# Kernel optimization log

Hardware: AMD Instinct MI355X
Metric: run time of the kernel (lower is better)

The kernel has to match this reference:

```python
import jax, jax.numpy as jnp
import numpy as np

B, S, D = 4, 2048, 512
QKD = 256
HID = 3 * D  # expansion_factor=3
EPS = 1e-5


def _ln(x, g, b):
    m = jnp.mean(x, axis=-1, keepdims=True)
    v = jnp.mean((x - m) ** 2, axis=-1, keepdims=True)
    return (x - m) * jax.lax.rsqrt(v + EPS) * g + b


def setup_inputs() -> dict:
    key = jax.random.key(0)
    ks = jax.random.split(key, 12)
    s = lambda fan: 1.0 / np.sqrt(fan)
    return {
        "x":  jax.random.normal(ks[0], (B, S, D), jnp.float32),
        "Wm": jax.random.uniform(ks[1], (D, D), jnp.float32, -s(D), s(D)),
        "bm": jnp.zeros((D,), jnp.float32),
        "g1": jnp.ones((D,), jnp.float32),
        "b1": jnp.zeros((D,), jnp.float32),
        "Wh": jax.random.uniform(ks[2], (2 * HID, D), jnp.float32, -s(D), s(D)),
        "bh": jnp.zeros((2 * HID,), jnp.float32),
        "Wq": jax.random.uniform(ks[3], (QKD, D), jnp.float32, -s(D), s(D)),
        "bq": jnp.zeros((QKD,), jnp.float32),
        "Wb": jax.random.normal(ks[4], (QKD, QKD), jnp.float32),
        "Wo": jax.random.uniform(ks[5], (D, HID), jnp.float32, -s(HID), s(HID)),
        "bo": jnp.zeros((D,), jnp.float32),
        "g2": jnp.ones((D,), jnp.float32),
        "b2": jnp.zeros((D,), jnp.float32),
    }


def reference(x, Wm, bm, g1, b1, Wh, bh, Wq, bq, Wb, Wo, bo, g2, b2):
    seq_len = x.shape[-2]
    memory = jnp.einsum('bsd,ed->bse', x, Wm) + bm
    normed = _ln(x + memory, g1, b1)
    h = jax.nn.relu(jnp.einsum('bsd,hd->bsh', normed, Wh) + bh)
    v, gate = h[..., :HID], h[..., HID:]
    Z = jax.nn.relu(jnp.einsum('bsd,qd->bsq', normed, Wq) + bq)  # [B,S,QKD]
    QK = jnp.einsum('bid,de,bje->bij', Z, Wb, Z) / seq_len
    A = jax.nn.relu(QK) ** 2  # relu^2 attention, no softmax
    V = jnp.einsum('bij,bjd->bid', A, v) * gate
    out = _ln(jnp.einsum('bsh,dh->bsd', V, Wo) + bo, g2, b2)
    return out + x
```

## Files before the change

### kernel.cpp

```cpp
#include <hip/hip_runtime.h>

typedef unsigned short u16;
typedef unsigned char u8;
typedef __attribute__((ext_vector_type(8))) short short8;
typedef __attribute__((ext_vector_type(4))) float f32x4;
typedef __attribute__((ext_vector_type(8))) int int8v;
typedef __attribute__((ext_vector_type(4))) int int4v;

#define LN_EPS 1e-5f
#define SCALE_A 4096.f
#define SCALE_V 8.f
#define INV_SCALE_AV (1.f/32768.f)
#define MX_ONE 0x7F7F7F7Fu

__device__ __forceinline__ u16 f2bf(float f){
    union { float f; unsigned u; } c; c.f = f;
    unsigned u = c.u + 0x7FFFu + ((c.u >> 16) & 1u);
    return (u16)(u >> 16);
}
__device__ __forceinline__ float bf2f(u16 h){
    union { unsigned u; float f; } c; c.u = ((unsigned)h) << 16;
    return c.f;
}
__device__ __forceinline__ u8 f2fp8(float f){
    int r = __builtin_amdgcn_cvt_pk_fp8_f32(f, 0.f, 0, false);
    return (u8)(r & 0xFF);
}

enum { EPI_NONE=0, EPI_BIAS_RES, EPI_RELUSQ };
enum { OT_F32=0, OT_BF16=1, OT_FP8=2 };

__device__ __forceinline__ void gl2lds16(const void* g, void* lds){
    __builtin_amdgcn_global_load_lds(
        (const __attribute__((address_space(1))) unsigned*)g,
        (__attribute__((address_space(3))) unsigned*)lds, 16, 0, 0);
}

template<int EPI, int OT>
__global__ __launch_bounds__(256)
void mgemm(const u16* __restrict__ A, const u16* __restrict__ B, void* __restrict__ Cv,
           int K, int lda, int ldb, int ldc,
           long sAb, long sBb, long sCb,
           const float* __restrict__ bias,
           const float* __restrict__ ext, int ldext,
           float scale)
{
    __shared__ u16 sA[2][4096];
    __shared__ u16 sB[2][4096];
    const int tid = threadIdx.x;
    const int m0 = blockIdx.y * 128, n0 = blockIdx.x * 128;
    const int z  = blockIdx.z;
    const u16* Az = A + (size_t)z * sAb;
    const u16* Bz = B + (size_t)z * sBb;

    const int lane = tid & 63, quad = lane >> 4, l15 = lane & 15;
    const int wave = tid >> 6;
    const int wm = (wave >> 1) * 64, wn = (wave & 1) * 64;

    const u16* gA[2]; const u16* gB[2]; int lo[2];
#pragma unroll
    for (int r = 0; r < 2; r++){
        const int c = tid + r * 256;
        gA[r] = Az + (size_t)(m0 + (c & 127)) * lda + (c >> 7) * 8;
        gB[r] = Bz + (size_t)(n0 + (c & 127)) * ldb + (c >> 7) * 8;
        lo[r] = ((tid & 192) + r * 256) * 16;
    }

    auto stage = [&](int buf, int k0){
#pragma unroll
        for (int r = 0; r < 2; r++){
            gl2lds16(gA[r] + k0, (char*)sA[buf] + lo[r]);
            gl2lds16(gB[r] + k0, (char*)sB[buf] + lo[r]);
        }
    };

    f32x4 acc[4][4];
#pragma unroll
    for (int i = 0; i < 4; i++)
#pragma unroll
        for (int j = 0; j < 4; j++) acc[i][j] = (f32x4){0.f,0.f,0.f,0.f};

    stage(0, 0);
    int buf = 0;
    for (int k0 = 0; k0 < K; k0 += 32){
        __syncthreads();
        if (k0 + 32 < K) stage(buf ^ 1, k0 + 32);
        const u16* fA = sA[buf] + quad * 1024 + (wm + l15) * 8;
        const u16* fB = sB[buf] + quad * 1024 + (wn + l15) * 8;
        short8 a[4], b[4];
#pragma unroll
        for (int t = 0; t < 4; t++){
            a[t] = *(const short8*)(fA + t * 128);
            b[t] = *(const short8*)(fB + t * 128);
        }
#pragma unroll
        for (int i = 0; i < 4; i++)
#pragma unroll
            for (int j = 0; j < 4; j++)
                acc[i][j] = __builtin_amdgcn_mfma_f32_16x16x32_bf16(a[i], b[j], acc[i][j], 0, 0, 0);
        buf ^= 1;
    }

    float* Cf = (float*)Cv; u16* Ch = (u16*)Cv; u8* C8 = (u8*)Cv;
    const size_t zc = (size_t)z * sCb;
#pragma unroll
    for (int i = 0; i < 4; i++){
#pragma unroll
        for (int j = 0; j < 4; j++){
            const int n = n0 + wn + j * 16 + l15;
            float bs = (EPI==EPI_BIAS_RES) ? bias[n] : 0.f;
#pragma unroll
            for (int r = 0; r < 4; r++){
                const int m = m0 + wm + i * 16 + quad * 4 + r;
                float v = acc[i][j][r] + bs;
                if (EPI==EPI_BIAS_RES)
                    v += ext[(size_t)m * ldext + n];
                if (EPI==EPI_RELUSQ){ float t = fmaxf(v * scale, 0.f); v = t * t * SCALE_A; }
                if (OT==OT_FP8)       C8[zc + (size_t)m * ldc + n] = f2fp8(v);
                else if (OT==OT_BF16) Ch[zc + (size_t)m * ldc + n] = f2bf(v);
                else                  Cf[zc + (size_t)m * ldc + n] = v;
            }
        }
    }
}

__global__ __launch_bounds__(256)
void mgemm_dual(const u16* __restrict__ Anrm, const u16* __restrict__ Wh,
                const u16* __restrict__ Wq,
                const float* __restrict__ bh, const float* __restrict__ bq,
                u8* __restrict__ v8, u16* __restrict__ gbf, u16* __restrict__ Zb)
{
    __shared__ u16 sA[2][4096];
    __shared__ u16 sB[2][4096];
    const int tid = threadIdx.x;
    const bool isZ = blockIdx.x >= 24;
    const u16* Bm = isZ ? Wq : Wh;
    const float* bias = isZ ? bq : bh;
    const int m0 = blockIdx.y * 128;
    const int n0 = (isZ ? (blockIdx.x - 24) : blockIdx.x) * 128;
    const int K = 512, lda = 512, ldb = 512;

    const int lane = tid & 63, quad = lane >> 4, l15 = lane & 15;
    const int wave = tid >> 6;
    const int wm = (wave >> 1) * 64, wn = (wave & 1) * 64;

    const u16* gA[2]; const u16* gB[2]; int lo[2];
#pragma unroll
    for (int r = 0; r < 2; r++){
        const int c = tid + r * 256;
        gA[r] = Anrm + (size_t)(m0 + (c & 127)) * lda + (c >> 7) * 8;
        gB[r] = Bm   + (size_t)(n0 + (c & 127)) * ldb + (c >> 7) * 8;
        lo[r] = ((tid & 192) + r * 256) * 16;
    }
    auto stage = [&](int buf, int k0){
#pragma unroll
        for (int r = 0; r < 2; r++){
            gl2lds16(gA[r] + k0, (char*)sA[buf] + lo[r]);
            gl2lds16(gB[r] + k0, (char*)sB[buf] + lo[r]);
        }
    };

    f32x4 acc[4][4];
#pragma unroll
    for (int i = 0; i < 4; i++)
#pragma unroll
        for (int j = 0; j < 4; j++) acc[i][j] = (f32x4){0.f,0.f,0.f,0.f};

    stage(0, 0);
    int buf = 0;
    for (int k0 = 0; k0 < K; k0 += 32){
        __syncthreads();
        if (k0 + 32 < K) stage(buf ^ 1, k0 + 32);
        const u16* fA = sA[buf] + quad * 1024 + (wm + l15) * 8;
        const u16* fB = sB[buf] + quad * 1024 + (wn + l15) * 8;
        short8 a[4], b[4];
#pragma unroll
        for (int t = 0; t < 4; t++){
            a[t] = *(const short8*)(fA + t * 128);
            b[t] = *(const short8*)(fB + t * 128);
        }
#pragma unroll
        for (int i = 0; i < 4; i++)
#pragma unroll
            for (int j = 0; j < 4; j++)
                acc[i][j] = __builtin_amdgcn_mfma_f32_16x16x32_bf16(a[i], b[j], acc[i][j], 0, 0, 0);
        buf ^= 1;
    }

#pragma unroll
    for (int i = 0; i < 4; i++){
#pragma unroll
        for (int j = 0; j < 4; j++){
            const int n = n0 + wn + j * 16 + l15;
            const float bs = bias[n];
#pragma unroll
            for (int r = 0; r < 4; r++){
                const int m = m0 + wm + i * 16 + quad * 4 + r;
                float v = fmaxf(acc[i][j][r] + bs, 0.f);
                if (isZ)            Zb[(size_t)m * 256 + n] = f2bf(v);
                else if (n < 1536)  v8[(size_t)m * 1536 + n] = f2fp8(v * SCALE_V);
                else                gbf[(size_t)m * 1536 + n - 1536] = f2bf(v);
            }
        }
    }
}

__global__ __launch_bounds__(256)
void mgemm8mx(const u8* __restrict__ A, const u8* __restrict__ B, u16* __restrict__ C,
              int K, int lda, int ldb, int ldc,
              long sAb, long sBb, long sCb,
              const u16* __restrict__ gate, int ldext, long sEb)
{
    __shared__ u8 sA[16384];
    __shared__ u8 sB[16384];
    const int tid = threadIdx.x;
    const int m0 = blockIdx.y * 128, n0 = blockIdx.x * 128;
    const int z  = blockIdx.z;
    const u8* Az = A + (size_t)z * sAb;
    const u8* Bz = B + (size_t)z * sBb;

    const int lane = tid & 63, quad = lane >> 4, l15 = lane & 15;
    const int wave = tid >> 6;
    const int wm = (wave >> 1) * 64, wn = (wave & 1) * 64;

    const u8* gA[4]; const u8* gB[4]; int lo[4];
#pragma unroll
    for (int p = 0; p < 4; p++){
        const int r = p * 32 + (tid >> 3);
        const int j = (tid & 7) ^ (r & 7);
        gA[p] = Az + (size_t)(m0 + r) * lda + j * 16;
        gB[p] = Bz + (size_t)(n0 + r) * ldb + j * 16;
        lo[p] = p * 4096 + wave * 1024;
    }

    f32x4 acc[4][4];
#pragma unroll
    for (int i = 0; i < 4; i++)
#pragma unroll
        for (int j = 0; j < 4; j++) acc[i][j] = (f32x4){0.f,0.f,0.f,0.f};

    for (int k0 = 0; k0 < K; k0 += 128){
#pragma unroll
        for (int p = 0; p < 4; p++){
            gl2lds16(gA[p] + k0, (char*)sA + lo[p]);
            gl2lds16(gB[p] + k0, (char*)sB + lo[p]);
        }
        __syncthreads();
        int8v a[4], b[4];
#pragma unroll
        for (int i = 0; i < 4; i++){
            const int m = wm + i * 16 + l15;
            const int4v a0 = *(const int4v*)(sA + m * 128 + ((2*quad    ) ^ (m & 7)) * 16);
            const int4v a1 = *(const int4v*)(sA + m * 128 + ((2*quad + 1) ^ (m & 7)) * 16);
            a[i] = (int8v){a0[0],a0[1],a0[2],a0[3],a1[0],a1[1],a1[2],a1[3]};
            const int n = wn + i * 16 + l15;
            const int4v b0 = *(const int4v*)(sB + n * 128 + ((2*quad    ) ^ (n & 7)) * 16);
            const int4v b1 = *(const int4v*)(sB + n * 128 + ((2*quad + 1) ^ (n & 7)) * 16);
            b[i] = (int8v){b0[0],b0[1],b0[2],b0[3],b1[0],b1[1],b1[2],b1[3]};
        }
#pragma unroll
        for (int i = 0; i < 4; i++)
#pragma unroll
            for (int j = 0; j < 4; j++)
                acc[i][j] = __builtin_amdgcn_mfma_scale_f32_16x16x128_f8f6f4(
                    a[i], b[j], acc[i][j], 0, 0, 0, MX_ONE, 0, MX_ONE);
        __syncthreads();
    }

    const size_t zc = (size_t)z * sCb;
#pragma unroll
    for (int i = 0; i < 4; i++){
#pragma unroll
        for (int j = 0; j < 4; j++){
            const int n = n0 + wn + j * 16 + l15;
#pragma unroll
            for (int r = 0; r < 4; r++){
                const int m = m0 + wm + i * 16 + quad * 4 + r;
                float v = acc[i][j][r] * INV_SCALE_AV
                        * bf2f(gate[(size_t)z * sEb + (size_t)m * ldext + n]);
                C[zc + (size_t)m * ldc + n] = f2bf(v);
            }
        }
    }
}

template<bool OUT_BF, bool POST_RES, int NSUM, bool PRE_RES>
__global__ __launch_bounds__(256)
void ln_k(const float* __restrict__ in, const float* __restrict__ g,
          const float* __restrict__ b, const float* __restrict__ res_post,
          const float* __restrict__ res_pre, const float* __restrict__ bias2,
          long pstride, void* __restrict__ out)
{
    const int row = blockIdx.x, tid = threadIdx.x;
    const size_t base = (size_t)row * 512 + tid * 2;
    float2 v = *(const float2*)(in + base);
#pragma unroll
    for (int p = 1; p < NSUM; p++){
        const float2 w = *(const float2*)(in + (size_t)p * pstride + base);
        v.x += w.x; v.y += w.y;
    }
    if (NSUM > 1){
        const float2 bb2 = *(const float2*)(bias2 + tid * 2);
        v.x += bb2.x; v.y += bb2.y;
    }
    if (PRE_RES){
        const float2 r = *(const float2*)(res_pre + base);
        v.x += r.x; v.y += r.y;
    }
    float s = v.x + v.y, ss = v.x * v.x + v.y * v.y;
#pragma unroll
    for (int off = 32; off > 0; off >>= 1){
        s  += __shfl_down(s,  off);
        ss += __shfl_down(ss, off);
    }
    __shared__ float sbuf[8], ssbuf[8];
    const int wid = tid >> 6, lane = tid & 63;
    if (lane == 0){ sbuf[wid] = s; ssbuf[wid] = ss; }
    __syncthreads();
    if (tid == 0){
        float S = 0.f, SS = 0.f;
#pragma unroll
        for (int i = 0; i < 4; i++){ S += sbuf[i]; SS += ssbuf[i]; }
        const float mean = S * (1.f/512.f);
        const float var  = SS * (1.f/512.f) - mean * mean;
        sbuf[4]  = mean;
        ssbuf[4] = rsqrtf(var + LN_EPS);
    }
    __syncthreads();
    const float mean = sbuf[4], rstd = ssbuf[4];
    const float2 gg = *(const float2*)(g + tid * 2);
    const float2 bb = *(const float2*)(b + tid * 2);
    float ox = (v.x - mean) * rstd * gg.x + bb.x;
    float oy = (v.y - mean) * rstd * gg.y + bb.y;
    if (POST_RES){
        const float2 r = *(const float2*)(res_post + base);
        ox += r.x; oy += r.y;
    }
    if (OUT_BF){
        unsigned pk = ((unsigned)f2bf(oy) << 16) | (unsigned)f2bf(ox);
        ((unsigned*)out)[(size_t)row * 256 + tid] = pk;
    } else {
        *(float2*)((float*)out + base) = make_float2(ox, oy);
    }
}

__global__ __launch_bounds__(256)
void castall_k(const float* __restrict__ x, const float* __restrict__ Wm,
               const float* __restrict__ Wh, const float* __restrict__ Wq,
               const float* __restrict__ Wo, const float* __restrict__ Wb,
               u16* __restrict__ xb, u16* __restrict__ Wmb, u16* __restrict__ Whb,
               u16* __restrict__ Wqb, u16* __restrict__ Wob, u16* __restrict__ WbT)
{
    const int i = blockIdx.x * 256 + threadIdx.x;
    if (i >= 1736704){
        const int j = i - 1736704;
        if (j < 65536){
            const int e = j >> 8, d = j & 255;
            WbT[e * 256 + d] = f2bf(Wb[d * 256 + e]);
        }
        return;
    }
    const float* src; u16* dst; int off;
    if      (i < 1048576){ src = x;  dst = xb;  off = i; }
    else if (i < 1114112){ src = Wm; dst = Wmb; off = i - 1048576; }
    else if (i < 1507328){ src = Wh; dst = Whb; off = i - 1114112; }
    else if (i < 1540096){ src = Wq; dst = Wqb; off = i - 1507328; }
    else                 { src = Wo; dst = Wob; off = i - 1540096; }
    const float4 v = ((const float4*)src)[off];
    ushort4 o; o.x = f2bf(v.x); o.y = f2bf(v.y); o.z = f2bf(v.z); o.w = f2bf(v.w);
    ((ushort4*)dst)[off] = o;
}

__global__ __launch_bounds__(256)
void tr8_k(const u8* __restrict__ v, u8* __restrict__ vT, int S, int HID){
    const int b = blockIdx.z;
    const int h0 = blockIdx.x * 64, s0 = blockIdx.y * 64;
    __shared__ u8 t[64][68];
    const u8* vb = v + (size_t)b * S * HID;
    u8* vTb = vT + (size_t)b * HID * S;
    const int tid = threadIdx.x;
#pragma unroll
    for (int i = 0; i < 4; i++){
        int idx = tid + i * 256;
        int r = idx >> 4, c4 = (idx & 15) * 4;
        uchar4 u = *(const uchar4*)(vb + (size_t)(s0 + r) * HID + h0 + c4);
        t[r][c4] = u.x; t[r][c4+1] = u.y; t[r][c4+2] = u.z; t[r][c4+3] = u.w;
    }
    __syncthreads();
#pragma unroll
    for (int i = 0; i < 4; i++){
        int idx = tid + i * 256;
        int r = idx >> 4, c4 = (idx & 15) * 4;
        uchar4 u;
        u.x = t[c4][r]; u.y = t[c4+1][r]; u.z = t[c4+2][r]; u.w = t[c4+3][r];
        *(uchar4*)(vTb + (size_t)(h0 + r) * S + s0 + c4) = u;
    }
}

extern "C" void kernel_launch(void* const* d_in, const int* in_sizes, int n_in,
                              void* d_out, int out_size, void* d_ws, size_t ws_size,
                              hipStream_t stream)
{
    const float* x  = (const float*)d_in[0];
    const float* Wm = (const float*)d_in[1];
    const float* bm = (const float*)d_in[2];
    const float* g1 = (const float*)d_in[3];
    const float* b1 = (const float*)d_in[4];
    const float* Wh = (const float*)d_in[5];
    const float* bh = (const float*)d_in[6];
    const float* Wq = (const float*)d_in[7];
    const float* bq = (const float*)d_in[8];
    const float* Wb = (const float*)d_in[9];
    const float* Wo = (const float*)d_in[10];
    const float* bo = (const float*)d_in[11];
    const float* g2 = (const float*)d_in[12];
    const float* b2 = (const float*)d_in[13];
    float* out = (float*)d_out;
    (void)in_sizes; (void)n_in; (void)out_size; (void)ws_size;

    const int Bn=4, S=2048, D=512, QKD=256, HID=1536, H2=3072;
    const int M = Bn * S;
    const long MD = (long)M * D;

    char* p = (char*)d_ws;
    auto alloc = [&](size_t bytes)->void*{ void* r = p; p += (bytes + 255) & ~(size_t)255; return r; };
    u16*  xbf  = (u16*) alloc((size_t)M*D*2);
    u16*  Wmbf = (u16*) alloc((size_t)D*D*2);
    u16*  Whbf = (u16*) alloc((size_t)H2*D*2);
    u16*  Wqbf = (u16*) alloc((size_t)QKD*D*2);
    u16*  Wobf = (u16*) alloc((size_t)D*HID*2);
    u16*  WbT  = (u16*) alloc((size_t)QKD*QKD*2);
    float* ybuf= (float*)alloc((size_t)MD*4*3);
    u16*  Zb   = (u16*) alloc((size_t)M*QKD*2);
    u16*  ZWbb = (u16*) alloc((size_t)M*QKD*2);
    u8*   v8   = (u8*)  alloc((size_t)M*HID);
    u16*  gbf  = (u16*) alloc((size_t)M*HID*2);
    u8*   vT8  = (u8*)  alloc((size_t)M*HID);
    u8*   A8   = (u8*)  alloc((size_t)M*S);
    u16*  Vgbf = (u16*) alloc((size_t)M*HID*2);
    u16*  nrm  = xbf;

    dim3 blk(256);

    castall_k<<<dim3(7040), blk, 0, stream>>>(x, Wm, Wh, Wq, Wo, Wb,
                                              xbf, Wmbf, Whbf, Wqbf, Wobf, WbT);
    mgemm<EPI_BIAS_RES,OT_F32><<<dim3(D/128, M/128, 1), blk, 0, stream>>>(
        xbf, Wmbf, ybuf, D, D, D, D, 0,0,0, bm, x, D, 1.f);
    ln_k<true,false,1,false><<<dim3(M), blk, 0, stream>>>(
        ybuf, g1, b1, nullptr, nullptr, nullptr, 0, nrm);
    mgemm_dual<<<dim3(26, M/128), blk, 0, stream>>>(
        nrm, Whbf, Wqbf, bh, bq, v8, gbf, Zb);
    mgemm<EPI_NONE,OT_BF16><<<dim3(QKD/128, M/128, 1), blk, 0, stream>>>(
        Zb, WbT, ZWbb, QKD, QKD, QKD, QKD, 0,0,0, nullptr, nullptr, 0, 1.f);
    mgemm<EPI_RELUSQ,OT_FP8><<<dim3(S/128, S/128, Bn), blk, 0, stream>>>(
        ZWbb, Zb, A8, QKD, QKD, QKD, S,
        (long)S*QKD, (long)S*QKD, (long)S*S,
        nullptr, nullptr, 0, 1.f/(float)S);
    tr8_k<<<dim3(HID/64, S/64, Bn), blk, 0, stream>>>(v8, vT8, S, HID);
    mgemm8mx<<<dim3(HID/128, S/128, Bn), blk, 0, stream>>>(
        A8, vT8, Vgbf, S, S, S, HID,
        (long)S*S, (long)HID*S, (long)S*HID,
        gbf, HID, (long)S*HID);
    mgemm<EPI_NONE,OT_F32><<<dim3(D/128, M/128, 3), blk, 0, stream>>>(
        Vgbf, Wobf, ybuf, HID/3, HID, HID, D, 512, 512, MD,
        nullptr, nullptr, 0, 1.f);
    ln_k<false,true,3,false><<<dim3(M), blk, 0, stream>>>(
        ybuf, g2, b2, x, nullptr, bo, MD, out);
}
```

Measured before the change: 341.7 us.

## Use single-buffered K=64 staging in bf16 GEMMs and reduce output split-K to 2

The two bf16 GEMM kernels drop the double-buffered K=32 pipeline. They now load a K=64 tile into one LDS buffer, synchronize, compute, then synchronize again before the next load. This halves the number of loop iterations and barriers, but global loads no longer overlap with MFMA work inside a block. The output projection split-K goes from 3 to 2 slices, which means a smaller partial-sum buffer and less reduction work in the final LayerNorm, at the cost of fewer blocks.

```diff
diff --git a/kernel.cpp b/kernel.cpp
--- a/kernel.cpp
+++ b/kernel.cpp
@@ -45,8 +45,8 @@
            const float* __restrict__ ext, int ldext,
            float scale)
 {
-    __shared__ u16 sA[2][4096];
-    __shared__ u16 sB[2][4096];
+    __shared__ u16 sA[8192];
+    __shared__ u16 sB[8192];
     const int tid = threadIdx.x;
     const int m0 = blockIdx.y * 128, n0 = blockIdx.x * 128;
     const int z  = blockIdx.z;
@@ -57,22 +57,14 @@
     const int wave = tid >> 6;
     const int wm = (wave >> 1) * 64, wn = (wave & 1) * 64;
 
-    const u16* gA[2]; const u16* gB[2]; int lo[2];
-#pragma unroll
-    for (int r = 0; r < 2; r++){
-        const int c = tid + r * 256;
-        gA[r] = Az + (size_t)(m0 + (c & 127)) * lda + (c >> 7) * 8;
-        gB[r] = Bz + (size_t)(n0 + (c & 127)) * ldb + (c >> 7) * 8;
-        lo[r] = ((tid & 192) + r * 256) * 16;
-    }
-
-    auto stage = [&](int buf, int k0){
-#pragma unroll
-        for (int r = 0; r < 2; r++){
-            gl2lds16(gA[r] + k0, (char*)sA[buf] + lo[r]);
-            gl2lds16(gB[r] + k0, (char*)sB[buf] + lo[r]);
-        }
-    };
+    const u16* gA[4]; const u16* gB[4]; int lo[4];
+#pragma unroll
+    for (int p = 0; p < 4; p++){
+        const int c = tid + p * 256;
+        gA[p] = Az + (size_t)(m0 + (c & 127)) * lda + (c >> 7) * 8;
+        gB[p] = Bz + (size_t)(n0 + (c & 127)) * ldb + (c >> 7) * 8;
+        lo[p] = ((tid & 192) + p * 256) * 16;
+    }
 
     f32x4 acc[4][4];
 #pragma unroll
@@ -80,25 +72,30 @@
 #pragma unroll
         for (int j = 0; j < 4; j++) acc[i][j] = (f32x4){0.f,0.f,0.f,0.f};
 
-    stage(0, 0);
-    int buf = 0;
-    for (int k0 = 0; k0 < K; k0 += 32){
-        __syncthreads();
-        if (k0 + 32 < K) stage(buf ^ 1, k0 + 32);
-        const u16* fA = sA[buf] + quad * 1024 + (wm + l15) * 8;
-        const u16* fB = sB[buf] + quad * 1024 + (wn + l15) * 8;
-        short8 a[4], b[4];
-#pragma unroll
-        for (int t = 0; t < 4; t++){
-            a[t] = *(const short8*)(fA + t * 128);
-            b[t] = *(const short8*)(fB + t * 128);
-        }
-#pragma unroll
-        for (int i = 0; i < 4; i++)
-#pragma unroll
-            for (int j = 0; j < 4; j++)
-                acc[i][j] = __builtin_amdgcn_mfma_f32_16x16x32_bf16(a[i], b[j], acc[i][j], 0, 0, 0);
-        buf ^= 1;
+    for (int k0 = 0; k0 < K; k0 += 64){
+#pragma unroll
+        for (int p = 0; p < 4; p++){
+            gl2lds16(gA[p] + k0, (char*)sA + lo[p]);
+            gl2lds16(gB[p] + k0, (char*)sB + lo[p]);
+        }
+        __syncthreads();
+#pragma unroll
+        for (int kb = 0; kb < 2; kb++){
+            const u16* fA = sA + (kb * 4 + quad) * 1024 + (wm + l15) * 8;
+            const u16* fB = sB + (kb * 4 + quad) * 1024 + (wn + l15) * 8;
+            short8 a[4], b[4];
+#pragma unroll
+            for (int t = 0; t < 4; t++){
+                a[t] = *(const short8*)(fA + t * 128);
+                b[t] = *(const short8*)(fB + t * 128);
+            }
+#pragma unroll
+            for (int i = 0; i < 4; i++)
+#pragma unroll
+                for (int j = 0; j < 4; j++)
+                    acc[i][j] = __builtin_amdgcn_mfma_f32_16x16x32_bf16(a[i], b[j], acc[i][j], 0, 0, 0);
+        }
+        __syncthreads();
     }
 
     float* Cf = (float*)Cv; u16* Ch = (u16*)Cv; u8* C8 = (u8*)Cv;
@@ -130,8 +127,8 @@
                 const float* __restrict__ bh, const float* __restrict__ bq,
                 u8* __restrict__ v8, u16* __restrict__ gbf, u16* __restrict__ Zb)
 {
-    __shared__ u16 sA[2][4096];
-    __shared__ u16 sB[2][4096];
+    __shared__ u16 sA[8192];
+    __shared__ u16 sB[8192];
     const int tid = threadIdx.x;
     const bool isZ = blockIdx.x >= 24;
     const u16* Bm = isZ ? Wq : Wh;
@@ -144,21 +141,14 @@
     const int wave = tid >> 6;
     const int wm = (wave >> 1) * 64, wn = (wave & 1) * 64;
 
-    const u16* gA[2]; const u16* gB[2]; int lo[2];
-#pragma unroll
-    for (int r = 0; r < 2; r++){
-        const int c = tid + r * 256;
-        gA[r] = Anrm + (size_t)(m0 + (c & 127)) * lda + (c >> 7) * 8;
-        gB[r] = Bm   + (size_t)(n0 + (c & 127)) * ldb + (c >> 7) * 8;
-        lo[r] = ((tid & 192) + r * 256) * 16;
-    }
-    auto stage = [&](int buf, int k0){
-#pragma unroll
-        for (int r = 0; r < 2; r++){
-            gl2lds16(gA[r] + k0, (char*)sA[buf] + lo[r]);
-            gl2lds16(gB[r] + k0, (char*)sB[buf] + lo[r]);
-        }
-    };
+    const u16* gA[4]; const u16* gB[4]; int lo[4];
+#pragma unroll
+    for (int p = 0; p < 4; p++){
+        const int c = tid + p * 256;
+        gA[p] = Anrm + (size_t)(m0 + (c & 127)) * lda + (c >> 7) * 8;
+        gB[p] = Bm   + (size_t)(n0 + (c & 127)) * ldb + (c >> 7) * 8;
+        lo[p] = ((tid & 192) + p * 256) * 16;
+    }
 
     f32x4 acc[4][4];
 #pragma unroll
@@ -166,25 +156,30 @@
 #pragma unroll
         for (int j = 0; j < 4; j++) acc[i][j] = (f32x4){0.f,0.f,0.f,0.f};
 
-    stage(0, 0);
-    int buf = 0;
-    for (int k0 = 0; k0 < K; k0 += 32){
-        __syncthreads();
-        if (k0 + 32 < K) stage(buf ^ 1, k0 + 32);
-        const u16* fA = sA[buf] + quad * 1024 + (wm + l15) * 8;
-        const u16* fB = sB[buf] + quad * 1024 + (wn + l15) * 8;
-        short8 a[4], b[4];
-#pragma unroll
-        for (int t = 0; t < 4; t++){
-            a[t] = *(const short8*)(fA + t * 128);
-            b[t] = *(const short8*)(fB + t * 128);
-        }
-#pragma unroll
-        for (int i = 0; i < 4; i++)
-#pragma unroll
-            for (int j = 0; j < 4; j++)
-                acc[i][j] = __builtin_amdgcn_mfma_f32_16x16x32_bf16(a[i], b[j], acc[i][j], 0, 0, 0);
-        buf ^= 1;
+    for (int k0 = 0; k0 < K; k0 += 64){
+#pragma unroll
+        for (int p = 0; p < 4; p++){
+            gl2lds16(gA[p] + k0, (char*)sA + lo[p]);
+            gl2lds16(gB[p] + k0, (char*)sB + lo[p]);
+        }
+        __syncthreads();
+#pragma unroll
+        for (int kb = 0; kb < 2; kb++){
+            const u16* fA = sA + (kb * 4 + quad) * 1024 + (wm + l15) * 8;
+            const u16* fB = sB + (kb * 4 + quad) * 1024 + (wn + l15) * 8;
+            short8 a[4], b[4];
+#pragma unroll
+            for (int t = 0; t < 4; t++){
+                a[t] = *(const short8*)(fA + t * 128);
+                b[t] = *(const short8*)(fB + t * 128);
+            }
+#pragma unroll
+            for (int i = 0; i < 4; i++)
+#pragma unroll
+                for (int j = 0; j < 4; j++)
+                    acc[i][j] = __builtin_amdgcn_mfma_f32_16x16x32_bf16(a[i], b[j], acc[i][j], 0, 0, 0);
+        }
+        __syncthreads();
     }
 
 #pragma unroll
@@ -430,7 +425,7 @@
     u16*  Wqbf = (u16*) alloc((size_t)QKD*D*2);
     u16*  Wobf = (u16*) alloc((size_t)D*HID*2);
     u16*  WbT  = (u16*) alloc((size_t)QKD*QKD*2);
-    float* ybuf= (float*)alloc((size_t)MD*4*3);
+    float* ybuf= (float*)alloc((size_t)MD*4*2);
     u16*  Zb   = (u16*) alloc((size_t)M*QKD*2);
     u16*  ZWbb = (u16*) alloc((size_t)M*QKD*2);
     u8*   v8   = (u8*)  alloc((size_t)M*HID);
@@ -461,9 +456,9 @@
         A8, vT8, Vgbf, S, S, S, HID,
         (long)S*S, (long)HID*S, (long)S*HID,
         gbf, HID, (long)S*HID);
-    mgemm<EPI_NONE,OT_F32><<<dim3(D/128, M/128, 3), blk, 0, stream>>>(
-        Vgbf, Wobf, ybuf, HID/3, HID, HID, D, 512, 512, MD,
+    mgemm<EPI_NONE,OT_F32><<<dim3(D/128, M/128, 2), blk, 0, stream>>>(
+        Vgbf, Wobf, ybuf, HID/2, HID, HID, D, 768, 768, MD,
         nullptr, nullptr, 0, 1.f);
-    ln_k<false,true,3,false><<<dim3(M), blk, 0, stream>>>(
+    ln_k<false,true,2,false><<<dim3(M), blk, 0, stream>>>(
         ybuf, g2, b2, x, nullptr, bo, MD, out);
 }
```

New measurement: 344.9 us. No clear change (+0.9%).
